# Optimization experiments

Hardware: AMD Instinct MI355X
Metric: run time of the kernel (lower is better)

## Reference

```python
import jax, jax.numpy as jnp
import numpy as np

B, NPG, IN_DIM, H, E = 128, 500, 3, 128, 512000
N = B * NPG
NEG = -1e9  # stands in for -inf masked fill; exp underflows to exactly 0 in fp32
BN_EPS = 1e-5


def setup_inputs() -> dict:
    key = jax.random.key(0)
    ks = jax.random.split(key, 40)
    rn = lambda k, shape: (jax.random.normal(k, shape, jnp.float32) * 0.05)
    x = jax.random.normal(ks[0], (N, IN_DIM), jnp.float32)
    g = jax.random.randint(ks[1], (E,), 0, B)
    src = jax.random.randint(ks[2], (E,), 0, NPG) + g * NPG
    dst = jax.random.randint(ks[3], (E,), 0, NPG) + g * NPG
    edge_index = jnp.stack([src, dst]).astype(jnp.int32)
    batch = (jnp.arange(N) // NPG).astype(jnp.int32)
    feasible_mask = jax.random.uniform(ks[4], (B, NPG, NPG)) < 0.1
    feasible_mask = feasible_mask.at[:, 0, 0].set(True)  # >=1 feasible action/graph
    return dict(
        x=x, edge_index=edge_index, batch=batch, feasible_mask=feasible_mask,
        gin_W1_0=rn(ks[5], (IN_DIM, H)), gin_b1_0=jnp.zeros((H,), jnp.float32),
        gin_g_0=jnp.ones((H,), jnp.float32), gin_be_0=jnp.zeros((H,), jnp.float32),
        gin_W2_0=rn(ks[6], (H, H)), gin_b2_0=jnp.zeros((H,), jnp.float32),
        gin_W1=rn(ks[7], (3, H, H)), gin_b1=jnp.zeros((3, H), jnp.float32),
        gin_g=jnp.ones((3, H), jnp.float32), gin_be=jnp.zeros((3, H), jnp.float32),
        gin_W2=rn(ks[8], (3, H, H)), gin_b2=jnp.zeros((3, H), jnp.float32),
        pol_W1_0=rn(ks[9], (2 * H, H)), pol_b1_0=jnp.zeros((H,), jnp.float32),
        pol_W2_0=rn(ks[10], (H, H)), pol_b2_0=jnp.zeros((H,), jnp.float32),
        pol_W1=rn(ks[11], (2, H, H)), pol_b1=jnp.zeros((2, H), jnp.float32),
        pol_W2=rn(ks[12], (2, H, H)), pol_b2=jnp.zeros((2, H), jnp.float32),
    )


def _gin_conv(h, src, dst, deg, W1, b1, g, be, W2, b2):
    # mean-aggregate neighbors (self loops already in edge list), eps=0
    agg = jax.ops.segment_sum(h[src], dst, num_segments=N) / deg[:, None]
    z = (h + agg) @ W1 + b1
    mu = jnp.mean(z, axis=0)
    var = jnp.var(z, axis=0)  # biased var, as torch BN training mode
    z = (z - mu) * jax.lax.rsqrt(var + BN_EPS) * g + be
    return jax.nn.relu(z) @ W2 + b2


def reference(x, edge_index, batch, feasible_mask,
              gin_W1_0, gin_b1_0, gin_g_0, gin_be_0, gin_W2_0, gin_b2_0,
              gin_W1, gin_b1, gin_g, gin_be, gin_W2, gin_b2,
              pol_W1_0, pol_b1_0, pol_W2_0, pol_b2_0,
              pol_W1, pol_b1, pol_W2, pol_b2):
    # add self loops
    loop = jnp.arange(N, dtype=edge_index.dtype)
    src = jnp.concatenate([edge_index[0], loop])
    dst = jnp.concatenate([edge_index[1], loop])
    deg = jnp.maximum(jax.ops.segment_sum(jnp.ones_like(src, jnp.float32), dst, num_segments=N), 1.0)

    h = _gin_conv(x, src, dst, deg, gin_W1_0, gin_b1_0, gin_g_0, gin_be_0, gin_W2_0, gin_b2_0)
    node_pool = h
    graph_pool = jax.ops.segment_sum(h, batch, num_segments=B) / NPG
    for l in range(3):
        h = _gin_conv(h, src, dst, deg, gin_W1[l], gin_b1[l], gin_g[l], gin_be[l], gin_W2[l], gin_b2[l])
        node_pool = node_pool + h
        graph_pool = graph_pool + jax.ops.segment_sum(h, batch, num_segments=B) / NPG

    # augment node embeds with their graph embed (graphs contiguous, equal size)
    a = jnp.concatenate([node_pool, graph_pool[batch]], axis=-1).reshape(B, NPG, 2 * H)
    a = jnp.tanh(a @ pol_W1_0 + pol_b1_0) @ pol_W2_0 + pol_b2_0
    for l in range(2):
        a = jnp.tanh(a @ pol_W1[l] + pol_b1[l]) @ pol_W2[l] + pol_b2[l]

    scores = jnp.einsum('bnd,bmd->bnm', a, a)                 # [B, n, n]
    scores = jnp.where(feasible_mask, scores, NEG)
    flat = scores.reshape(B, NPG * NPG)
    logp_all = jax.nn.log_softmax(flat, axis=-1)
    actions_id = jax.random.categorical(jax.random.key(42), flat, axis=-1)  # [B]
    log_prob = jnp.take_along_axis(logp_all, actions_id[:, None], axis=1)[:, 0]
    return actions_id, log_prob
```

## Files before the change

### kernel.cpp

```cpp
#include <hip/hip_runtime.h>
#include <float.h>

#define NN 64000
#define BB 128
#define NPGc 500
#define EE 512000

__device__ __forceinline__ unsigned rotl32(unsigned x, unsigned r){ return (x<<r)|(x>>(32u-r)); }

__device__ __forceinline__ unsigned threefry_bits(unsigned idx){
  unsigned x0 = 0u, x1 = idx;
  const unsigned ks0 = 0u, ks1 = 42u, ks2 = 0u ^ 42u ^ 0x1BD11BDAu;
  x0 += ks0; x1 += ks1;
#define RND(r) { x0 += x1; x1 = rotl32(x1, r); x1 ^= x0; }
  RND(13u) RND(15u) RND(26u) RND(6u)   x0 += ks1; x1 += ks2 + 1u;
  RND(17u) RND(29u) RND(16u) RND(24u)  x0 += ks2; x1 += ks0 + 2u;
  RND(13u) RND(15u) RND(26u) RND(6u)   x0 += ks0; x1 += ks1 + 3u;
  RND(17u) RND(29u) RND(16u) RND(24u)  x0 += ks1; x1 += ks2 + 4u;
  RND(13u) RND(15u) RND(26u) RND(6u)   x0 += ks2; x1 += ks0 + 5u;
#undef RND
  return x0 ^ x1;
}

__device__ __forceinline__ float gumbel_of(unsigned idx){
  unsigned bits = threefry_bits(idx);
  float f = __uint_as_float((bits >> 9) | 0x3f800000u) - 1.0f;
  const float TINY = 1.17549435e-38f;
  float u = fmaxf(TINY, f + TINY);
  return -logf(-logf(u));
}

__device__ __forceinline__ float fast_tanh(float x){
  return 1.0f - 2.0f/(__expf(2.0f*x) + 1.0f);
}

__global__ void maskdet_kernel(const unsigned* __restrict__ m, int* __restrict__ flag){
  if (threadIdx.x == 0){
    int isbool = 0;
    for (int i=0;i<256;i++){ if (m[i] > 1u){ isbool = 1; break; } }
    *flag = isbool;
  }
}

__global__ __launch_bounds__(256)
void maskprep_kernel(const unsigned char* __restrict__ mu8src, const int* __restrict__ mi32src,
                     const int* __restrict__ mflag, unsigned char* __restrict__ mn8,
                     unsigned char* __restrict__ mt8){
  __shared__ unsigned char tile[64][65];
  const int b = blockIdx.y;
  const int rt = blockIdx.x >> 3, ct = blockIdx.x & 7;
  const int t = threadIdx.x;
  const int lane = t & 63, rr = t >> 6;
  const int isbool = *mflag;
#pragma unroll
  for (int p=0;p<16;p++){
    int row = rt*64 + p*4 + rr;
    int col = ct*64 + lane;
    unsigned char v = 0;
    if (row < NPGc && col < NPGc){
      size_t off = (size_t)b*250000 + (size_t)row*500 + col;
      v = isbool ? mu8src[off] : (unsigned char)(mi32src[off] != 0);
      if (!isbool) mn8[off] = v;
    }
    tile[p*4+rr][lane] = v;
  }
  __syncthreads();
#pragma unroll
  for (int p=0;p<16;p++){
    int orow = ct*64 + p*4 + rr;
    int ocol = rt*64 + lane;
    if (orow < NPGc && ocol < NPGc){
      size_t off = (size_t)b*250000 + (size_t)orow*500 + ocol;
      mt8[off] = tile[lane][p*4+rr];
    }
  }
}

__global__ void count_kernel(const int* __restrict__ dst, int* __restrict__ cnt){
  int e = blockIdx.x*256 + threadIdx.x;
  if (e < EE) atomicAdd(&cnt[dst[e]], 1);
}

__global__ __launch_bounds__(1024)
void scan_kernel(const int* __restrict__ cnt, int* __restrict__ off, int* __restrict__ cur){
  __shared__ int part[1024];
  int tid = threadIdx.x;
  const int chunk = 63;
  int base = tid*chunk;
  int sum = 0;
  for (int i=0;i<chunk;i++){ int n = base+i; if (n < NN) sum += cnt[n]; }
  part[tid] = sum;
  __syncthreads();
  for (int d=1; d<1024; d<<=1){
    int v = (tid >= d) ? part[tid-d] : 0;
    __syncthreads();
    part[tid] += v;
    __syncthreads();
  }
  int run = part[tid] - sum;
  for (int i=0;i<chunk;i++){
    int n = base+i;
    if (n < NN){ off[n] = run; cur[n] = run; run += cnt[n]; }
  }
  if (tid == 1023) off[NN] = run;
}

__global__ void fill_kernel(const int* __restrict__ src, const int* __restrict__ dst,
                            int* __restrict__ cur, int* __restrict__ csr){
  int e = blockIdx.x*256 + threadIdx.x;
  if (e < EE){
    int d = dst[e];
    int p = atomicAdd(&cur[d], 1);
    csr[p] = src[e];
  }
}

__global__ void agg3_kernel(const float* __restrict__ x, const int* __restrict__ off,
                            const int* __restrict__ csr, const int* __restrict__ cnt,
                            float* __restrict__ xin0){
  int n = blockIdx.x*256 + threadIdx.x;
  if (n >= NN) return;
  float a0 = x[n*3], a1 = x[n*3+1], a2 = x[n*3+2];
  float s0 = a0, s1 = a1, s2 = a2;
  int e1 = off[n+1];
  for (int e = off[n]; e < e1; ++e){
    int s = csr[e];
    s0 += x[s*3]; s1 += x[s*3+1]; s2 += x[s*3+2];
  }
  float di = 1.0f/(float)(cnt[n]+1);
  xin0[n*3]   = a0 + s0*di;
  xin0[n*3+1] = a1 + s1*di;
  xin0[n*3+2] = a2 + s2*di;
}

__global__ __launch_bounds__(256)
void agg128_kernel(const float* __restrict__ h, const int* __restrict__ off,
                   const int* __restrict__ csr, const int* __restrict__ cnt,
                   float* __restrict__ xin){
  const int nb = gridDim.x;
  const int per = nb >> 3;
  int bid = (blockIdx.x % 8)*per + (blockIdx.x >> 3);
  int w = (bid*256 + (int)threadIdx.x) >> 6;
  int lane = threadIdx.x & 63;
  if (w >= NN) return;
  const float* hn = h + (size_t)w*128;
  float a0 = hn[lane], a1 = hn[lane+64];
  float s0 = a0, s1 = a1;
  int e0 = off[w], e1 = off[w+1];
  for (int e = e0; e < e1; ++e){
    int s = csr[e];
    const float* hs = h + (size_t)s*128;
    s0 += hs[lane]; s1 += hs[lane+64];
  }
  float di = 1.0f/(float)(cnt[w]+1);
  xin[(size_t)w*128 + lane]      = a0 + s0*di;
  xin[(size_t)w*128 + lane + 64] = a1 + s1*di;
}

__global__ __launch_bounds__(256)
void z0_kernel(const float* __restrict__ xin0, const float* __restrict__ W,
               const float* __restrict__ bias, float* __restrict__ z,
               float* __restrict__ stats){
  __shared__ float xr[192];
  __shared__ float ssum[128], ssq[128];
  int t = threadIdx.x;
  int row0 = blockIdx.x*64;
  if (t < 192) xr[t] = xin0[(size_t)row0*3 + t];
  if (t < 128){ ssum[t]=0.f; ssq[t]=0.f; }
  int f = t & 127, rg = t >> 7;
  float w0 = W[f], w1 = W[128+f], w2 = W[256+f], bb = bias[f];
  __syncthreads();
  float s = 0.f, q = 0.f;
  for (int i=0;i<32;i++){
    int r = rg*32 + i;
    float y = bb + xr[r*3]*w0 + xr[r*3+1]*w1 + xr[r*3+2]*w2;
    z[(size_t)(row0+r)*128 + f] = y;
    s += y; q += y*y;
  }
  atomicAdd(&ssum[f], s); atomicAdd(&ssq[f], q);
  __syncthreads();
  if (t < 128){ atomicAdd(&stats[t], ssum[t]); atomicAdd(&stats[128+t], ssq[t]); }
}

__global__ void bnfin_kernel(float* __restrict__ stats, const float* __restrict__ g,
                             const float* __restrict__ be, float* __restrict__ bnbuf){
  int f = threadIdx.x;
  float mu  = stats[f]     * (1.0f/NN);
  float var = stats[128+f] * (1.0f/NN) - mu*mu;
  float rsv = rsqrtf(var + 1e-5f);
  float sc  = g[f]*rsv;
  bnbuf[f]      = sc;
  bnbuf[128+f]  = be[f] - mu*sc;
  stats[f] = 0.f; stats[128+f] = 0.f;
}

template<int K, bool CATF, bool BNF, bool TANHF, bool STATSF, int POOLM>
__global__ __launch_bounds__(256, 2)
void linear_kernel(const float* X, const float* __restrict__ X2,
                   const float* __restrict__ W, const float* __restrict__ bias,
                   float* Y,
                   const float* __restrict__ bnsc, const float* __restrict__ bnsh,
                   float* __restrict__ stats, float* __restrict__ pool){
  __shared__ __align__(16) float xs[32][132];
  __shared__ __align__(16) float ws[32][132];
  __shared__ float ssum[128], ssq[128];
  const int t = threadIdx.x;
  const int row0 = blockIdx.x*128;
  const int cg = t & 15, rg = t >> 4;
  const int c0 = cg*8, r0 = rg*8;
  float acc[8][8];
#pragma unroll
  for (int r=0;r<8;r++)
#pragma unroll
    for (int c=0;c<8;c++) acc[r][c]=0.f;
  if (STATSF && t < 128){ ssum[t]=0.f; ssq[t]=0.f; }

  for (int kc=0; kc<K; kc+=32){
    __syncthreads();
#pragma unroll
    for (int i=0;i<4;i++){
      int task = t + 256*i;
      int n = task >> 3, k4 = task & 7;
      int gk = kc + k4*4;
      int row = row0 + n;
      float4 v;
      if (CATF){
        if (gk < 128) v = *(const float4*)(X  + (size_t)row*128 + gk);
        else          v = *(const float4*)(X2 + (size_t)(row/NPGc)*128 + (gk-128));
      } else {
        v = *(const float4*)(X + (size_t)row*K + gk);
      }
      if (BNF){
        float4 sc4 = *(const float4*)(bnsc + gk);
        float4 sh4 = *(const float4*)(bnsh + gk);
        v.x = fmaxf(0.f, v.x*sc4.x + sh4.x);
        v.y = fmaxf(0.f, v.y*sc4.y + sh4.y);
        v.z = fmaxf(0.f, v.z*sc4.z + sh4.z);
        v.w = fmaxf(0.f, v.w*sc4.w + sh4.w);
      }
      xs[k4*4+0][n] = v.x; xs[k4*4+1][n] = v.y;
      xs[k4*4+2][n] = v.z; xs[k4*4+3][n] = v.w;
    }
#pragma unroll
    for (int i=0;i<4;i++){
      int task = t + 256*i;
      int k = task >> 5, c4 = task & 31;
      float4 v = *(const float4*)(W + (size_t)(kc+k)*128 + c4*4);
      *(float4*)&ws[k][c4*4] = v;
    }
    __syncthreads();
#pragma unroll
    for (int k=0;k<32;k++){
      float4 xa = *(const float4*)&xs[k][r0];
      float4 xb = *(const float4*)&xs[k][r0+4];
      float4 wa = *(const float4*)&ws[k][c0];
      float4 wb = *(const float4*)&ws[k][c0+4];
      float xv[8] = {xa.x,xa.y,xa.z,xa.w,xb.x,xb.y,xb.z,xb.w};
      float wv[8] = {wa.x,wa.y,wa.z,wa.w,wb.x,wb.y,wb.z,wb.w};
#pragma unroll
      for (int r=0;r<8;r++)
#pragma unroll
        for (int c=0;c<8;c++)
          acc[r][c] += xv[r]*wv[c];
    }
  }
  float4 ba = *(const float4*)(bias + c0);
  float4 bb2 = *(const float4*)(bias + c0 + 4);
  float bv[8] = {ba.x,ba.y,ba.z,ba.w,bb2.x,bb2.y,bb2.z,bb2.w};
  float sc8[8], sq8[8];
#pragma unroll
  for (int c=0;c<8;c++){ sc8[c]=0.f; sq8[c]=0.f; }
#pragma unroll
  for (int r=0;r<8;r++){
    int n = row0 + r0 + r;
    float y[8];
#pragma unroll
    for (int c=0;c<8;c++){
      float v = acc[r][c] + bv[c];
      if (TANHF) v = fast_tanh(v);
      y[c] = v;
    }
    float4 y0; y0.x=y[0]; y0.y=y[1]; y0.z=y[2]; y0.w=y[3];
    float4 y1; y1.x=y[4]; y1.y=y[5]; y1.z=y[6]; y1.w=y[7];
    *(float4*)(Y + (size_t)n*128 + c0)     = y0;
    *(float4*)(Y + (size_t)n*128 + c0 + 4) = y1;
    if (POOLM == 1){
      *(float4*)(pool + (size_t)n*128 + c0)     = y0;
      *(float4*)(pool + (size_t)n*128 + c0 + 4) = y1;
    } else if (POOLM == 2){
      float4 p0 = *(const float4*)(pool + (size_t)n*128 + c0);
      float4 p1 = *(const float4*)(pool + (size_t)n*128 + c0 + 4);
      p0.x+=y[0]; p0.y+=y[1]; p0.z+=y[2]; p0.w+=y[3];
      p1.x+=y[4]; p1.y+=y[5]; p1.z+=y[6]; p1.w+=y[7];
      *(float4*)(pool + (size_t)n*128 + c0)     = p0;
      *(float4*)(pool + (size_t)n*128 + c0 + 4) = p1;
    }
    if (STATSF){
#pragma unroll
      for (int c=0;c<8;c++){ sc8[c]+=y[c]; sq8[c]+=y[c]*y[c]; }
    }
  }
  if (STATSF){
#pragma unroll
    for (int c=0;c<8;c++){
      atomicAdd(&ssum[c0+c], sc8[c]);
      atomicAdd(&ssq[c0+c],  sq8[c]);
    }
    __syncthreads();
    if (t < 128){
      atomicAdd(&stats[t],     ssum[t]);
      atomicAdd(&stats[128+t], ssq[t]);
    }
  }
}

__global__ __launch_bounds__(512)
void gpool_kernel(const float* __restrict__ pool, float* __restrict__ gpool){
  __shared__ float red[4][128];
  int b = blockIdx.x;
  int f = threadIdx.x & 127, part = threadIdx.x >> 7;
  const float* p = pool + (size_t)b*NPGc*128 + f;
  int rbeg = part*125, rend = rbeg + 125;
  float s = 0.f;
  for (int i=rbeg;i<rend;i++) s += p[(size_t)i*128];
  red[part][f] = s;
  __syncthreads();
  if (part == 0){
    float tot = ((red[0][f] + red[1][f]) + red[2][f]) + red[3][f];
    gpool[(size_t)b*128 + f] = tot * (1.0f/NPGc);
  }
}

#define QCAP 1024
#define NPAIR 36

__global__ __launch_bounds__(256)
void scores_tri_kernel(const float* __restrict__ A, const unsigned char* __restrict__ mn8,
                       const unsigned char* __restrict__ mt8, float* __restrict__ partials){
  __shared__ __align__(16) float as[128][68];
  __shared__ __align__(16) float bs[32][68];
  __shared__ float qs[QCAP];
  __shared__ int   qi[QCAP];
  __shared__ int   qcnt;
  float* rm  = qs;
  float* rs_ = qs + 256;
  float* rv  = qs + 512;
  float* rsc = qs + 768;
  int*   ri  = qi;
  const int t = threadIdx.x;
  const int xcd = blockIdx.x & 7;
  const int within = blockIdx.x >> 3;
  const int b = xcd*16 + within/NPAIR;
  int pidx = within % NPAIR, tn = 0;
  while (pidx >= 8 - tn){ pidx -= 8 - tn; tn++; }
  const int tm = tn + pidx;
  const int pair = within % NPAIR;
  const bool diag = (tn == tm);
  const int n0 = tn*64, m0 = tm*64;
  const int cgc = t & 15, rgc = t >> 4;
  const int r0_ = rgc*4, c0 = cgc*4;
  const float* Ab = A + (size_t)b*NPGc*128;
  const unsigned gbase = (unsigned)b*250000u;
  if (t == 0) qcnt = 0;

#pragma unroll
  for (int i=0;i<32;i++){
    int idx = t + 256*i;
    int k = idx & 127, r = idx >> 7;
    int n = n0 + r;
    as[k][r] = (n < NPGc) ? Ab[(size_t)n*128 + k] : 0.f;
  }

  float acc[4][4];
#pragma unroll
  for (int i2=0;i2<4;i2++)
#pragma unroll
    for (int j=0;j<4;j++) acc[i2][j]=0.f;

  for (int kc=0;kc<4;kc++){
    __syncthreads();
#pragma unroll
    for (int i=0;i<8;i++){
      int idx = t + 256*i;
      int kk = idx & 31, c = idx >> 5;
      int m = m0 + c;
      bs[kk][c] = (m < NPGc) ? Ab[(size_t)m*128 + kc*32 + kk] : 0.f;
    }
    __syncthreads();
#pragma unroll
    for (int kk=0;kk<32;kk++){
      float4 av = *(const float4*)&as[kc*32+kk][r0_];
      float4 bv4 = *(const float4*)&bs[kk][c0];
      float a_[4] = {av.x,av.y,av.z,av.w};
      float b_[4] = {bv4.x,bv4.y,bv4.z,bv4.w};
#pragma unroll
      for (int i2=0;i2<4;i2++)
#pragma unroll
        for (int j=0;j<4;j++)
          acc[i2][j] += a_[i2]*b_[j];
    }
  }

  float mrun = -1e30f, srun = 0.f, bval = -FLT_MAX, bsc = 0.f;
  int bidx = 0x7FFFFFFF;
  const int mbase = m0 + c0;
  const bool colok = (mbase < NPGc);
#pragma unroll
  for (int i2=0;i2<4;i2++){
    int n = n0 + r0_ + i2;
    bool rowok = colok && (n < NPGc);
    bool fn[4] = {false,false,false,false};
    bool fm[4] = {false,false,false,false};
    if (rowok){
      size_t moff = (size_t)b*250000 + (size_t)n*500 + (size_t)mbase;
      uchar4 mk = *(const uchar4*)(mn8 + moff);
      fn[0]=mk.x!=0; fn[1]=mk.y!=0; fn[2]=mk.z!=0; fn[3]=mk.w!=0;
      uchar4 tk = *(const uchar4*)(mt8 + moff);
      fm[0]=tk.x!=0; fm[1]=tk.y!=0; fm[2]=tk.z!=0; fm[3]=tk.w!=0;
    }
    float cntj[4], sj[4];
    bool pn[4], pm[4];
#pragma unroll
    for (int j=0;j<4;j++){
      int m = mbase + j;
      bool mok = rowok && (m < NPGc);
      bool keep = mok && (!diag || m >= n);
      bool isde = (n == m);
      float cnt = 0.f; bool a1=false, a2=false;
      if (keep){
        if (isde){ cnt = fn[j] ? 1.f : 0.f; a1 = fn[j]; }
        else { cnt = (fn[j]?1.f:0.f) + (fm[j]?1.f:0.f); a1 = fn[j]; a2 = fm[j]; }
      }
      cntj[j]=cnt; pn[j]=a1; pm[j]=a2;
      sj[j] = (cnt > 0.f) ? acc[i2][j] : -1e30f;
    }
    float tmx = fmaxf(fmaxf(sj[0],sj[1]), fmaxf(sj[2],sj[3]));
    float nm = fmaxf(mrun, tmx);
    float add = 0.f;
#pragma unroll
    for (int j=0;j<4;j++) add += cntj[j]*__expf(sj[j] - nm);
    srun = srun*__expf(mrun - nm) + add;
    mrun = nm;
#pragma unroll
    for (int j=0;j<4;j++){
      int m = mbase + j;
      if (pn[j] || pm[j]){
        float s = acc[i2][j];
#pragma unroll
        for (int d=0;d<2;d++){
          bool doit = d ? pm[j] : pn[j];
          if (doit){
            int lidx = d ? (m*500 + n) : (n*500 + m);
            int slot = atomicAdd(&qcnt, 1);
            if (slot < QCAP){ qs[slot] = s; qi[slot] = lidx; }
            else {
              float g = gumbel_of(gbase + (unsigned)lidx);
              float val = s + g;
              if (val > bval || (val == bval && lidx < bidx)){ bval = val; bidx = lidx; bsc = s; }
            }
          }
        }
      }
    }
  }
  __syncthreads();
  int qn = qcnt; if (qn > QCAP) qn = QCAP;
  for (int i = t; i < qn; i += 256){
    float s = qs[i]; int idx = qi[i];
    float g = gumbel_of(gbase + (unsigned)idx);
    float val = s + g;
    if (val > bval || (val == bval && idx < bidx)){ bval = val; bidx = idx; bsc = s; }
  }
  __syncthreads();
  rm[t]=mrun; rs_[t]=srun; rv[t]=bval; ri[t]=bidx; rsc[t]=bsc;
  __syncthreads();
  for (int offr=128; offr>0; offr>>=1){
    if (t < offr){
      float m1 = rm[t], s1 = rs_[t];
      float m2 = rm[t+offr], s2 = rs_[t+offr];
      float M = fmaxf(m1, m2);
      float S = s1*expf(m1-M) + s2*expf(m2-M);
      rm[t] = M; rs_[t] = S;
      float v2 = rv[t+offr]; int i2_ = ri[t+offr];
      if (v2 > rv[t] || (v2 == rv[t] && i2_ < ri[t])){ rv[t]=v2; ri[t]=i2_; rsc[t]=rsc[t+offr]; }
    }
    __syncthreads();
  }
  if (t == 0){
    float* p = partials + ((size_t)b*NPAIR + pair)*8;
    p[0]=rm[0]; p[1]=rs_[0]; p[2]=rv[0]; p[3]=(float)ri[0]; p[4]=rsc[0];
  }
}

__global__ void finalize_kernel(const float* __restrict__ partials, float* __restrict__ out){
  int b = threadIdx.x;
  float M = -1e30f, S = 0.f, BV = -FLT_MAX, BS = 0.f;
  int BI = 0x7FFFFFFF;
  for (int tp=0; tp<NPAIR; tp++){
    const float* p = partials + ((size_t)b*NPAIR + tp)*8;
    float m = p[0], s = p[1], v = p[2]; int i = (int)p[3]; float sc2 = p[4];
    float nM = fmaxf(M, m);
    S = S*expf(M-nM) + s*expf(m-nM);
    M = nM;
    if (v > BV || (v == BV && i < BI)){ BV = v; BI = i; BS = sc2; }
  }
  out[b]      = (float)BI;
  out[BB + b] = BS - (M + logf(S));
}

__global__ void maskptr_kernel(const int* __restrict__ mflag,
                               const unsigned char* srcu8, const unsigned char* mn8buf,
                               const unsigned char** __restrict__ outp){
  if (threadIdx.x == 0) *outp = (*mflag) ? srcu8 : mn8buf;
}

__global__ void noop_kernel(){}

extern "C" void kernel_launch(void* const* d_in, const int* in_sizes, int n_in,
                              void* d_out, int out_size, void* d_ws, size_t ws_size,
                              hipStream_t stream){
  const float* x        = (const float*)d_in[0];
  const int*   eidx     = (const int*)d_in[1];
  const void*  maskp    = d_in[3];
  const float* gin_W1_0 = (const float*)d_in[4];
  const float* gin_b1_0 = (const float*)d_in[5];
  const float* gin_g_0  = (const float*)d_in[6];
  const float* gin_be_0 = (const float*)d_in[7];
  const float* gin_W2_0 = (const float*)d_in[8];
  const float* gin_b2_0 = (const float*)d_in[9];
  const float* gin_W1   = (const float*)d_in[10];
  const float* gin_b1   = (const float*)d_in[11];
  const float* gin_g    = (const float*)d_in[12];
  const float* gin_be   = (const float*)d_in[13];
  const float* gin_W2   = (const float*)d_in[14];
  const float* gin_b2   = (const float*)d_in[15];
  const float* pol_W1_0 = (const float*)d_in[16];
  const float* pol_b1_0 = (const float*)d_in[17];
  const float* pol_W2_0 = (const float*)d_in[18];
  const float* pol_b2_0 = (const float*)d_in[19];
  const float* pol_W1   = (const float*)d_in[20];
  const float* pol_b1   = (const float*)d_in[21];
  const float* pol_W2   = (const float*)d_in[22];
  const float* pol_b2   = (const float*)d_in[23];
  float* out = (float*)d_out;

  char* p = (char*)d_ws;
  auto carve = [&](size_t bytes) -> void* {
    void* r = (void*)p; p += (bytes + 255) & ~(size_t)255; return r;
  };
  float* hbuf  = (float*)carve((size_t)NN*128*4);
  float* xin   = (float*)carve((size_t)NN*128*4);
  float* pool  = (float*)carve((size_t)NN*128*4);
  float* xin0  = (float*)carve((size_t)NN*3*4);
  float* gpool = (float*)carve((size_t)BB*128*4);
  float* stats = (float*)carve(256*4);
  float* bnbuf = (float*)carve(256*4);
  float* partials = (float*)carve((size_t)BB*NPAIR*8*4);
  int* cnt = (int*)carve((size_t)NN*4);
  int* off = (int*)carve((size_t)(NN+1)*4);
  int* cur = (int*)carve((size_t)NN*4);
  int* csr = (int*)carve((size_t)EE*4);
  int* mflag = (int*)carve(256);
  unsigned char* mn8 = (unsigned char*)carve((size_t)BB*250000);
  unsigned char* mt8 = (unsigned char*)carve((size_t)BB*250000);

  const int* srcp = eidx;
  const int* dstp = eidx + EE;

  maskdet_kernel<<<1, 64, 0, stream>>>((const unsigned*)maskp, mflag);
  {
    dim3 mg(64, BB);
    maskprep_kernel<<<mg, 256, 0, stream>>>((const unsigned char*)maskp, (const int*)maskp,
                                            mflag, mn8, mt8);
  }
  {
    struct L { static __global__ void k(const int* f, const unsigned char* s, unsigned char* d){
    } };
  }

  hipMemsetAsync(cnt, 0, (size_t)NN*4, stream);
  count_kernel<<<(EE+255)/256, 256, 0, stream>>>(dstp, cnt);
  scan_kernel<<<1, 1024, 0, stream>>>(cnt, off, cur);
  fill_kernel<<<(EE+255)/256, 256, 0, stream>>>(srcp, dstp, cur, csr);

  agg3_kernel<<<(NN+255)/256, 256, 0, stream>>>(x, off, csr, cnt, xin0);
  hipMemsetAsync(stats, 0, 256*4, stream);
  z0_kernel<<<NN/64, 256, 0, stream>>>(xin0, gin_W1_0, gin_b1_0, xin, stats);
  bnfin_kernel<<<1, 128, 0, stream>>>(stats, gin_g_0, gin_be_0, bnbuf);
  linear_kernel<128,false,true,false,false,1><<<NN/128, 256, 0, stream>>>(
      xin, nullptr, gin_W2_0, gin_b2_0, hbuf, bnbuf, bnbuf+128, nullptr, pool);

  for (int l=0; l<3; l++){
    agg128_kernel<<<NN/4, 256, 0, stream>>>(hbuf, off, csr, cnt, xin);
    linear_kernel<128,false,false,false,true,0><<<NN/128, 256, 0, stream>>>(
        xin, nullptr, gin_W1 + (size_t)l*16384, gin_b1 + l*128, xin,
        nullptr, nullptr, stats, nullptr);
    bnfin_kernel<<<1, 128, 0, stream>>>(stats, gin_g + l*128, gin_be + l*128, bnbuf);
    linear_kernel<128,false,true,false,false,2><<<NN/128, 256, 0, stream>>>(
        xin, nullptr, gin_W2 + (size_t)l*16384, gin_b2 + l*128, hbuf,
        bnbuf, bnbuf+128, nullptr, pool);
  }

  gpool_kernel<<<BB, 512, 0, stream>>>(pool, gpool);
  linear_kernel<256,true,false,true,false,0><<<NN/128, 256, 0, stream>>>(
      pool, gpool, pol_W1_0, pol_b1_0, hbuf, nullptr, nullptr, nullptr, nullptr);
  linear_kernel<128,false,false,false,false,0><<<NN/128, 256, 0, stream>>>(
      hbuf, nullptr, pol_W2_0, pol_b2_0, xin, nullptr, nullptr, nullptr, nullptr);
  linear_kernel<128,false,false,true,false,0><<<NN/128, 256, 0, stream>>>(
      xin, nullptr, pol_W1, pol_b1, hbuf, nullptr, nullptr, nullptr, nullptr);
  linear_kernel<128,false,false,false,false,0><<<NN/128, 256, 0, stream>>>(
      hbuf, nullptr, pol_W2, pol_b2, xin, nullptr, nullptr, nullptr, nullptr);
  linear_kernel<128,false,false,true,false,0><<<NN/128, 256, 0, stream>>>(
      xin, nullptr, pol_W1 + 16384, pol_b1 + 128, hbuf, nullptr, nullptr, nullptr, nullptr);
  linear_kernel<128,false,false,false,false,0><<<NN/128, 256, 0, stream>>>(
      hbuf, nullptr, pol_W2 + 16384, pol_b2 + 128, xin, nullptr, nullptr, nullptr, nullptr);

  scores_tri_kernel<<<8*16*NPAIR, 256, 0, stream>>>(xin, mn8, mt8, partials);
  finalize_kernel<<<1, BB, 0, stream>>>(partials, out);
}
```

Measured before the change: 1.438 ms.

## Parallelize CSR scan, fuse first aggregation, skew LDS tiles, warp-aggregate queue atomics

Replaces the single-block serial prefix scan with a three-pass multi-block scan. It folds the 3-feature neighbor aggregation into the first linear kernel and drops a separate kernel and buffer. It skews the shared-memory layout of the GEMM tiles to reduce bank conflicts on float4 reads, and replaces per-element atomics on the candidate queue with one wavefront-aggregated atomic via ballot/popcount. The mask prep now always writes the normalized mask copy, which adds extra writes when the input is already bool.

```diff
diff --git a/kernel.cpp b/kernel.cpp
--- a/kernel.cpp
+++ b/kernel.cpp
@@ -5,6 +5,9 @@
 #define BB 128
 #define NPGc 500
 #define EE 512000
+
+#define SKW(c) ((c) + (((c)>>3)<<2))
+#define LW 188
 
 __device__ __forceinline__ unsigned rotl32(unsigned x, unsigned r){ return (x<<r)|(x>>(32u-r)); }
 
@@ -60,7 +63,7 @@
     if (row < NPGc && col < NPGc){
       size_t off = (size_t)b*250000 + (size_t)row*500 + col;
       v = isbool ? mu8src[off] : (unsigned char)(mi32src[off] != 0);
-      if (!isbool) mn8[off] = v;
+      mn8[off] = v;
     }
     tile[p*4+rr][lane] = v;
   }
@@ -81,28 +84,43 @@
   if (e < EE) atomicAdd(&cnt[dst[e]], 1);
 }
 
-__global__ __launch_bounds__(1024)
-void scan_kernel(const int* __restrict__ cnt, int* __restrict__ off, int* __restrict__ cur){
-  __shared__ int part[1024];
-  int tid = threadIdx.x;
-  const int chunk = 63;
-  int base = tid*chunk;
-  int sum = 0;
-  for (int i=0;i<chunk;i++){ int n = base+i; if (n < NN) sum += cnt[n]; }
-  part[tid] = sum;
-  __syncthreads();
-  for (int d=1; d<1024; d<<=1){
-    int v = (tid >= d) ? part[tid-d] : 0;
-    __syncthreads();
-    part[tid] += v;
-    __syncthreads();
-  }
-  int run = part[tid] - sum;
-  for (int i=0;i<chunk;i++){
-    int n = base+i;
-    if (n < NN){ off[n] = run; cur[n] = run; run += cnt[n]; }
-  }
-  if (tid == 1023) off[NN] = run;
+__global__ void scanA_kernel(const int* __restrict__ cnt, int* __restrict__ bsum){
+  __shared__ int red[256];
+  int t = threadIdx.x;
+  red[t] = cnt[blockIdx.x*256 + t];
+  __syncthreads();
+  for (int s=128;s>0;s>>=1){
+    if (t < s) red[t] += red[t+s];
+    __syncthreads();
+  }
+  if (t == 0) bsum[blockIdx.x] = red[0];
+}
+
+__global__ void scanB_kernel(const int* __restrict__ bsum, int* __restrict__ boff){
+  if (threadIdx.x == 0){
+    int run = 0;
+    for (int i=0;i<250;i++){ boff[i] = run; run += bsum[i]; }
+    boff[250] = run;
+  }
+}
+
+__global__ void scanC_kernel(const int* __restrict__ cnt, const int* __restrict__ boff,
+                             int* __restrict__ off, int* __restrict__ cur){
+  __shared__ int red[256];
+  int t = threadIdx.x;
+  int n = blockIdx.x*256 + t;
+  int v = cnt[n];
+  red[t] = v;
+  __syncthreads();
+  for (int d=1; d<256; d<<=1){
+    int x = (t >= d) ? red[t-d] : 0;
+    __syncthreads();
+    red[t] += x;
+    __syncthreads();
+  }
+  int excl = red[t] - v + boff[blockIdx.x];
+  off[n] = excl; cur[n] = excl;
+  if (n == NN-1) off[NN] = excl + v;
 }
 
 __global__ void fill_kernel(const int* __restrict__ src, const int* __restrict__ dst,
@@ -113,24 +131,6 @@
     int p = atomicAdd(&cur[d], 1);
     csr[p] = src[e];
   }
-}
-
-__global__ void agg3_kernel(const float* __restrict__ x, const int* __restrict__ off,
-                            const int* __restrict__ csr, const int* __restrict__ cnt,
-                            float* __restrict__ xin0){
-  int n = blockIdx.x*256 + threadIdx.x;
-  if (n >= NN) return;
-  float a0 = x[n*3], a1 = x[n*3+1], a2 = x[n*3+2];
-  float s0 = a0, s1 = a1, s2 = a2;
-  int e1 = off[n+1];
-  for (int e = off[n]; e < e1; ++e){
-    int s = csr[e];
-    s0 += x[s*3]; s1 += x[s*3+1]; s2 += x[s*3+2];
-  }
-  float di = 1.0f/(float)(cnt[n]+1);
-  xin0[n*3]   = a0 + s0*di;
-  xin0[n*3+1] = a1 + s1*di;
-  xin0[n*3+2] = a2 + s2*di;
 }
 
 __global__ __launch_bounds__(256)
@@ -158,14 +158,24 @@
 }
 
 __global__ __launch_bounds__(256)
-void z0_kernel(const float* __restrict__ xin0, const float* __restrict__ W,
-               const float* __restrict__ bias, float* __restrict__ z,
-               float* __restrict__ stats){
+void z0_kernel(const float* __restrict__ x, const int* __restrict__ off,
+               const int* __restrict__ csr, const int* __restrict__ cnt,
+               const float* __restrict__ W, const float* __restrict__ bias,
+               float* __restrict__ z, float* __restrict__ stats){
   __shared__ float xr[192];
   __shared__ float ssum[128], ssq[128];
   int t = threadIdx.x;
   int row0 = blockIdx.x*64;
-  if (t < 192) xr[t] = xin0[(size_t)row0*3 + t];
+  if (t < 192){
+    int nl = t/3, f = t - nl*3;
+    int n = row0 + nl;
+    float a = x[n*3+f];
+    float s = a;
+    int e1 = off[n+1];
+    for (int e = off[n]; e < e1; ++e) s += x[csr[e]*3 + f];
+    float di = 1.0f/(float)(cnt[n]+1);
+    xr[t] = a + s*di;
+  }
   if (t < 128){ ssum[t]=0.f; ssq[t]=0.f; }
   int f = t & 127, rg = t >> 7;
   float w0 = W[f], w1 = W[128+f], w2 = W[256+f], bb = bias[f];
@@ -201,13 +211,14 @@
                    float* Y,
                    const float* __restrict__ bnsc, const float* __restrict__ bnsh,
                    float* __restrict__ stats, float* __restrict__ pool){
-  __shared__ __align__(16) float xs[32][132];
-  __shared__ __align__(16) float ws[32][132];
+  __shared__ __align__(16) float xs[32][LW];
+  __shared__ __align__(16) float ws[32][LW];
   __shared__ float ssum[128], ssq[128];
   const int t = threadIdx.x;
   const int row0 = blockIdx.x*128;
   const int cg = t & 15, rg = t >> 4;
   const int c0 = cg*8, r0 = rg*8;
+  const int skr0 = SKW(r0), skc0 = SKW(c0);
   float acc[8][8];
 #pragma unroll
   for (int r=0;r<8;r++)
@@ -238,23 +249,24 @@
         v.z = fmaxf(0.f, v.z*sc4.z + sh4.z);
         v.w = fmaxf(0.f, v.w*sc4.w + sh4.w);
       }
-      xs[k4*4+0][n] = v.x; xs[k4*4+1][n] = v.y;
-      xs[k4*4+2][n] = v.z; xs[k4*4+3][n] = v.w;
+      int ns = SKW(n);
+      xs[k4*4+0][ns] = v.x; xs[k4*4+1][ns] = v.y;
+      xs[k4*4+2][ns] = v.z; xs[k4*4+3][ns] = v.w;
     }
 #pragma unroll
     for (int i=0;i<4;i++){
       int task = t + 256*i;
       int k = task >> 5, c4 = task & 31;
       float4 v = *(const float4*)(W + (size_t)(kc+k)*128 + c4*4);
-      *(float4*)&ws[k][c4*4] = v;
+      *(float4*)&ws[k][c4*4 + ((c4>>1)<<2)] = v;
     }
     __syncthreads();
 #pragma unroll
     for (int k=0;k<32;k++){
-      float4 xa = *(const float4*)&xs[k][r0];
-      float4 xb = *(const float4*)&xs[k][r0+4];
-      float4 wa = *(const float4*)&ws[k][c0];
-      float4 wb = *(const float4*)&ws[k][c0+4];
+      float4 xa = *(const float4*)&xs[k][skr0];
+      float4 xb = *(const float4*)&xs[k][skr0+4];
+      float4 wa = *(const float4*)&ws[k][skc0];
+      float4 wb = *(const float4*)&ws[k][skc0+4];
       float xv[8] = {xa.x,xa.y,xa.z,xa.w,xb.x,xb.y,xb.z,xb.w};
       float wv[8] = {wa.x,wa.y,wa.z,wa.w,wb.x,wb.y,wb.z,wb.w};
 #pragma unroll
@@ -348,6 +360,7 @@
   float* rsc = qs + 768;
   int*   ri  = qi;
   const int t = threadIdx.x;
+  const int lane = t & 63;
   const int xcd = blockIdx.x & 7;
   const int within = blockIdx.x >> 3;
   const int b = xcd*16 + within/NPAIR;
@@ -444,14 +457,20 @@
 #pragma unroll
     for (int j=0;j<4;j++){
       int m = mbase + j;
-      if (pn[j] || pm[j]){
-        float s = acc[i2][j];
-#pragma unroll
-        for (int d=0;d<2;d++){
-          bool doit = d ? pm[j] : pn[j];
-          if (doit){
+      float s = acc[i2][j];
+#pragma unroll
+      for (int d=0;d<2;d++){
+        bool want = d ? pm[j] : pn[j];
+        unsigned long long mb = __ballot(want);
+        if (mb){
+          int cntw = __popcll(mb);
+          int pos  = __popcll(mb & ((1ull<<lane)-1ull));
+          int basew = 0;
+          if (lane == 0) basew = atomicAdd(&qcnt, cntw);
+          basew = __shfl(basew, 0);
+          if (want){
             int lidx = d ? (m*500 + n) : (n*500 + m);
-            int slot = atomicAdd(&qcnt, 1);
+            int slot = basew + pos;
             if (slot < QCAP){ qs[slot] = s; qi[slot] = lidx; }
             else {
               float g = gumbel_of(gbase + (unsigned)lidx);
@@ -507,14 +526,6 @@
   out[b]      = (float)BI;
   out[BB + b] = BS - (M + logf(S));
 }
-
-__global__ void maskptr_kernel(const int* __restrict__ mflag,
-                               const unsigned char* srcu8, const unsigned char* mn8buf,
-                               const unsigned char** __restrict__ outp){
-  if (threadIdx.x == 0) *outp = (*mflag) ? srcu8 : mn8buf;
-}
-
-__global__ void noop_kernel(){}
 
 extern "C" void kernel_launch(void* const* d_in, const int* in_sizes, int n_in,
                               void* d_out, int out_size, void* d_ws, size_t ws_size,
@@ -551,15 +562,16 @@
   float* hbuf  = (float*)carve((size_t)NN*128*4);
   float* xin   = (float*)carve((size_t)NN*128*4);
   float* pool  = (float*)carve((size_t)NN*128*4);
-  float* xin0  = (float*)carve((size_t)NN*3*4);
   float* gpool = (float*)carve((size_t)BB*128*4);
   float* stats = (float*)carve(256*4);
   float* bnbuf = (float*)carve(256*4);
   float* partials = (float*)carve((size_t)BB*NPAIR*8*4);
-  int* cnt = (int*)carve((size_t)NN*4);
-  int* off = (int*)carve((size_t)(NN+1)*4);
-  int* cur = (int*)carve((size_t)NN*4);
-  int* csr = (int*)carve((size_t)EE*4);
+  int* cnt  = (int*)carve((size_t)NN*4);
+  int* off  = (int*)carve((size_t)(NN+1)*4);
+  int* cur  = (int*)carve((size_t)NN*4);
+  int* csr  = (int*)carve((size_t)EE*4);
+  int* bsum = (int*)carve(256*4);
+  int* boff = (int*)carve(256*4);
   int* mflag = (int*)carve(256);
   unsigned char* mn8 = (unsigned char*)carve((size_t)BB*250000);
   unsigned char* mt8 = (unsigned char*)carve((size_t)BB*250000);
@@ -573,19 +585,16 @@
     maskprep_kernel<<<mg, 256, 0, stream>>>((const unsigned char*)maskp, (const int*)maskp,
                                             mflag, mn8, mt8);
   }
-  {
-    struct L { static __global__ void k(const int* f, const unsigned char* s, unsigned char* d){
-    } };
-  }
 
   hipMemsetAsync(cnt, 0, (size_t)NN*4, stream);
   count_kernel<<<(EE+255)/256, 256, 0, stream>>>(dstp, cnt);
-  scan_kernel<<<1, 1024, 0, stream>>>(cnt, off, cur);
+  scanA_kernel<<<NN/256, 256, 0, stream>>>(cnt, bsum);
+  scanB_kernel<<<1, 64, 0, stream>>>(bsum, boff);
+  scanC_kernel<<<NN/256, 256, 0, stream>>>(cnt, boff, off, cur);
   fill_kernel<<<(EE+255)/256, 256, 0, stream>>>(srcp, dstp, cur, csr);
 
-  agg3_kernel<<<(NN+255)/256, 256, 0, stream>>>(x, off, csr, cnt, xin0);
   hipMemsetAsync(stats, 0, 256*4, stream);
-  z0_kernel<<<NN/64, 256, 0, stream>>>(xin0, gin_W1_0, gin_b1_0, xin, stats);
+  z0_kernel<<<NN/64, 256, 0, stream>>>(x, off, csr, cnt, gin_W1_0, gin_b1_0, xin, stats);
   bnfin_kernel<<<1, 128, 0, stream>>>(stats, gin_g_0, gin_be_0, bnbuf);
   linear_kernel<128,false,true,false,false,1><<<NN/128, 256, 0, stream>>>(
       xin, nullptr, gin_W2_0, gin_b2_0, hbuf, bnbuf, bnbuf+128, nullptr, pool);
```

Result: faster. 1.325 ms (-7.9%).
